# Kernel tuning notes

Measured on AMD Instinct MI355X. Metric: run time of the kernel, lower is better.

Reference implementation:

```python
import jax, jax.numpy as jnp
import numpy as np

# Complete binary Huffman tree: V leaves, V-1 internal nodes, heap-indexed
# (node 0 = root, leaf i lives at heap index V-1+i, parent(n) = (n-1)//2).
V = 32768     # vocab size (leaves)
D = 15        # path depth = log2(V) internal nodes per leaf
DM = 1024     # input word-vector dim
B = 8         # batch of input word vectors
T = 1024      # target ids per batch item


def _build_paths():
    """paths[i, l] = heap index of the l-th internal node (leaf-to-root) on leaf i's path."""
    n = np.arange(V, dtype=np.int64) + (V - 1)  # leaf heap indices
    paths = np.zeros((V, D), dtype=np.int32)
    for lvl in range(D):
        n = (n - 1) // 2
        paths[:, lvl] = n
    return jnp.asarray(paths)


def setup_inputs() -> dict:
    key = jax.random.key(0)
    k1, k2, k3 = jax.random.split(key, 3)
    x = jax.random.normal(k1, (B, DM), dtype=jnp.float32)
    ids = jax.random.randint(k2, (B, T), 0, V)
    W = jax.random.normal(k3, (V - 1, DM), dtype=jnp.float32) * 0.02  # stacked Linear(DM,1) weights
    b = jnp.zeros((V - 1,), dtype=jnp.float32)                        # stacked Linear biases
    return {"x": x, "ids": ids, "paths": _build_paths(), "W": W, "b": b}


def reference(x, ids, paths, W, b):
    # node_idx: [B, T, D] internal-node heap indices along each target's path
    node_idx = paths[ids]
    Wp = W[node_idx]                 # [B, T, D, DM] gathered per-node weight rows
    bp = b[node_idx]                 # [B, T, D]
    # per-node Linear + bias: logit = w_node . x + b_node
    logits = jnp.einsum('btdk,bk->btd', Wp, x) + bp
    # product of sigmoid branch probabilities along the path -> [B, T]
    return jnp.prod(jax.nn.sigmoid(logits), axis=-1)
```

## Files before the change

### kernel.cpp

```cpp
#include <hip/hip_runtime.h>
#include <math.h>

#define V 32768
#define D 15
#define DM 1024
#define B 8
#define T 1024
#define NNODES (V - 1)

__global__ __launch_bounds__(256) void hsm_logits_kernel(
    const float* __restrict__ x,
    const float* __restrict__ W,
    const float* __restrict__ bias,
    float* __restrict__ sig)
{
    __shared__ float4 xs[B * DM / 4];

    const float4* x4 = (const float4*)x;
    for (int i = threadIdx.x; i < B * DM / 4; i += 256) xs[i] = x4[i];
    __syncthreads();

    const int wave = threadIdx.x >> 6;
    const int lane = threadIdx.x & 63;
    const int row0 = (blockIdx.x * 4 + wave) * 2;
    if (row0 >= NNODES) return;
    const bool two = (row0 + 1) < NNODES;

    const float4* w0 = (const float4*)(W + (size_t)row0 * DM);
    const float4* w1 = (const float4*)(W + (size_t)(two ? row0 + 1 : row0) * DM);

    float acc0[B], acc1[B];
    #pragma unroll
    for (int b = 0; b < B; b++) { acc0[b] = 0.f; acc1[b] = 0.f; }

    #pragma unroll
    for (int k = 0; k < 4; k++) {
        const float4 a = w0[k * 64 + lane];
        const float4 c = w1[k * 64 + lane];
        #pragma unroll
        for (int b = 0; b < B; b++) {
            const float4 xv = xs[b * (DM / 4) + k * 64 + lane];
            acc0[b] += a.x * xv.x + a.y * xv.y + a.z * xv.z + a.w * xv.w;
            acc1[b] += c.x * xv.x + c.y * xv.y + c.z * xv.z + c.w * xv.w;
        }
    }

    #pragma unroll
    for (int off = 32; off > 0; off >>= 1) {
        #pragma unroll
        for (int b = 0; b < B; b++) {
            acc0[b] += __shfl_down(acc0[b], off, 64);
            acc1[b] += __shfl_down(acc1[b], off, 64);
        }
    }

    if (lane == 0) {
        const float bb0 = bias[row0];
        #pragma unroll
        for (int b = 0; b < B; b++) {
            const float z = acc0[b] + bb0;
            sig[(size_t)row0 * B + b] = 1.f / (1.f + expf(-z));
        }
        if (two) {
            const float bb1 = bias[row0 + 1];
            #pragma unroll
            for (int b = 0; b < B; b++) {
                const float z = acc1[b] + bb1;
                sig[(size_t)(row0 + 1) * B + b] = 1.f / (1.f + expf(-z));
            }
        }
    }
}

__global__ __launch_bounds__(256) void hsm_prod_kernel(
    const int* __restrict__ ids,
    const int* __restrict__ paths,
    const float* __restrict__ sig,
    float* __restrict__ out)
{
    const int i = blockIdx.x * blockDim.x + threadIdx.x;
    if (i >= B * T) return;
    const int b = i / T;
    const int id = ids[i];
    const int* p = paths + (size_t)id * D;
    float prod = 1.f;
    #pragma unroll
    for (int d = 0; d < D; d++) {
        prod *= sig[(size_t)p[d] * B + b];
    }
    out[i] = prod;
}

extern "C" void kernel_launch(void* const* d_in, const int* in_sizes, int n_in,
                              void* d_out, int out_size, void* d_ws, size_t ws_size,
                              hipStream_t stream) {
    const float* x     = (const float*)d_in[0];
    const int*   ids   = (const int*)d_in[1];
    const int*   paths = (const int*)d_in[2];
    const float* W     = (const float*)d_in[3];
    const float* bias  = (const float*)d_in[4];
    float* out = (float*)d_out;
    float* sig = (float*)d_ws;

    const int rows_per_block = 8;
    const int grid1 = (NNODES + rows_per_block - 1) / rows_per_block;
    hsm_logits_kernel<<<grid1, 256, 0, stream>>>(x, W, bias, sig);

    const int grid2 = (B * T + 255) / 256;
    hsm_prod_kernel<<<grid2, 256, 0, stream>>>(ids, paths, sig, out);
}
```

Before: 212.3 us.

## Process eight weight rows per wave with butterfly transpose-reduction

Each wave now computes dot products for eight weight rows instead of two. The x values are loaded from shared memory once per chunk and reused across all eight rows. The per-row shuffle-down reductions are replaced by a recursive-halving xor butterfly, so each lane ends with one (row, batch) result, and all 64 lanes write sigmoid outputs in parallel instead of lane 0 alone. The kernel now holds 64 accumulators per thread, which raises register pressure; the launch-bounds occupancy hint is set to 3.

```diff
diff --git a/kernel.cpp b/kernel.cpp
--- a/kernel.cpp
+++ b/kernel.cpp
@@ -7,8 +7,9 @@
 #define B 8
 #define T 1024
 #define NNODES (V - 1)
+#define R 8
 
-__global__ __launch_bounds__(256) void hsm_logits_kernel(
+__global__ __launch_bounds__(256, 3) void hsm_logits_kernel(
     const float* __restrict__ x,
     const float* __restrict__ W,
     const float* __restrict__ bias,
@@ -17,58 +18,61 @@
     __shared__ float4 xs[B * DM / 4];
 
     const float4* x4 = (const float4*)x;
+    #pragma unroll
     for (int i = threadIdx.x; i < B * DM / 4; i += 256) xs[i] = x4[i];
     __syncthreads();
 
     const int wave = threadIdx.x >> 6;
     const int lane = threadIdx.x & 63;
-    const int row0 = (blockIdx.x * 4 + wave) * 2;
+    const int row0 = (blockIdx.x * 4 + wave) * R;
     if (row0 >= NNODES) return;
-    const bool two = (row0 + 1) < NNODES;
 
-    const float4* w0 = (const float4*)(W + (size_t)row0 * DM);
-    const float4* w1 = (const float4*)(W + (size_t)(two ? row0 + 1 : row0) * DM);
+    const float4* Wb = (const float4*)W;
 
-    float acc0[B], acc1[B];
+    float acc[R * B];
     #pragma unroll
-    for (int b = 0; b < B; b++) { acc0[b] = 0.f; acc1[b] = 0.f; }
+    for (int i = 0; i < R * B; i++) acc[i] = 0.f;
 
     #pragma unroll
-    for (int k = 0; k < 4; k++) {
-        const float4 a = w0[k * 64 + lane];
-        const float4 c = w1[k * 64 + lane];
+    for (int j = 0; j < 4; j++) {
+        const int u = j * 64 + lane;
+        float4 xv[B];
         #pragma unroll
-        for (int b = 0; b < B; b++) {
-            const float4 xv = xs[b * (DM / 4) + k * 64 + lane];
-            acc0[b] += a.x * xv.x + a.y * xv.y + a.z * xv.z + a.w * xv.w;
-            acc1[b] += c.x * xv.x + c.y * xv.y + c.z * xv.z + c.w * xv.w;
+        for (int b = 0; b < B; b++) xv[b] = xs[b * 256 + u];
+        #pragma unroll
+        for (int r = 0; r < R; r++) {
+            int row = row0 + r;
+            if (row > NNODES - 1) row = NNODES - 1;
+            const float4 wv = Wb[(size_t)row * 256 + u];
+            #pragma unroll
+            for (int b = 0; b < B; b++) {
+                acc[r * 8 + b] += wv.x * xv[b].x + wv.y * xv[b].y +
+                                  wv.z * xv[b].z + wv.w * xv[b].w;
+            }
         }
     }
 
     #pragma unroll
-    for (int off = 32; off > 0; off >>= 1) {
+    for (int m = 1, n = R * B; m <= 32; m <<= 1, n >>= 1) {
         #pragma unroll
-        for (int b = 0; b < B; b++) {
-            acc0[b] += __shfl_down(acc0[b], off, 64);
-            acc1[b] += __shfl_down(acc1[b], off, 64);
+        for (int i = 0; i < 64; i++) {
+            if (i < n / 2) {
+                const float lo = acc[2 * i];
+                const float hi = acc[2 * i + 1];
+                const float send = (lane & m) ? lo : hi;
+                const float keep = (lane & m) ? hi : lo;
+                const float recv = __shfl_xor(send, m, 64);
+                acc[i] = keep + recv;
+            }
         }
     }
 
-    if (lane == 0) {
-        const float bb0 = bias[row0];
-        #pragma unroll
-        for (int b = 0; b < B; b++) {
-            const float z = acc0[b] + bb0;
-            sig[(size_t)row0 * B + b] = 1.f / (1.f + expf(-z));
-        }
-        if (two) {
-            const float bb1 = bias[row0 + 1];
-            #pragma unroll
-            for (int b = 0; b < B; b++) {
-                const float z = acc1[b] + bb1;
-                sig[(size_t)(row0 + 1) * B + b] = 1.f / (1.f + expf(-z));
-            }
-        }
+    const int r = lane >> 3;
+    const int b = lane & 7;
+    const int row = row0 + r;
+    if (row < NNODES) {
+        const float z = acc[0] + bias[row];
+        sig[(size_t)row * B + b] = 1.f / (1.f + expf(-z));
     }
 }
 
@@ -102,7 +106,7 @@
     float* out = (float*)d_out;
     float* sig = (float*)d_ws;
 
-    const int rows_per_block = 8;
+    const int rows_per_block = 4 * R;
     const int grid1 = (NNODES + rows_per_block - 1) / rows_per_block;
     hsm_logits_kernel<<<grid1, 256, 0, stream>>>(x, W, bias, sig);
 
```

Result: slower. 228.5 us (+7.6%).
